# Kernel optimization log

Hardware: AMD Instinct MI355X
Metric: run time of the kernel (lower is better)

The kernel has to match this reference:

```python
import jax, jax.numpy as jnp
import numpy as np

B, D, K, V = 8192, 64, 200, 100000
EPS = 1e-5


def setup_inputs() -> dict:
    key = jax.random.key(0)
    ks = jax.random.split(key, 16)
    n = lambda k, s, sc=1.0: jax.random.normal(k, s, dtype=jnp.float32) * sc
    sw = 0.05  # weight scale for numeric stability
    inp = {
        'v_embed': n(ks[0], (V, D)),
        'embeds_u_1': n(ks[1], (B, D)),
        'embeds_u_2': n(ks[2], (B, D)),
        'embeds_u_3': n(ks[3], (B, D)),
        'embeds_u_4': n(ks[4], (B, D)),
        'embeds_v': n(ks[5], (B, D)),
        'w_ur1_w': n(ks[6], (D, D), sw), 'w_ur1_b': jnp.zeros((D,), jnp.float32),
        'w_ur2_w': n(ks[7], (D, D), sw), 'w_ur2_b': jnp.zeros((D,), jnp.float32),
        'w_vr1_w': n(ks[8], (D, D), sw), 'w_vr1_b': jnp.zeros((D,), jnp.float32),
        'w_vr2_w': n(ks[9], (D, D), sw), 'w_vr2_b': jnp.zeros((D,), jnp.float32),
        'w_uv1_w': n(ks[10], (2 * D, D), sw), 'w_uv1_b': jnp.zeros((D,), jnp.float32),
        'w_uv2_w': n(ks[11], (D, 16), sw), 'w_uv2_b': jnp.zeros((16,), jnp.float32),
        'w_uv3_w': n(ks[12], (16, 1), sw), 'w_uv3_b': jnp.zeros((1,), jnp.float32),
        'nodes_v': jax.random.randint(ks[13], (B,), 0, V),
        'nbr_idx': jax.random.randint(ks[14], (B, K), 0, V),
        'nbr_len': jax.random.randint(ks[15], (B,), 1, K),
    }
    for name, dim in (('bn1', D), ('bn2', D), ('bn3', D), ('bn4', 16)):
        inp[name + '_g'] = jnp.ones((dim,), jnp.float32)
        inp[name + '_b'] = jnp.zeros((dim,), jnp.float32)
        inp[name + '_m'] = jnp.zeros((dim,), jnp.float32)
        inp[name + '_v'] = jnp.ones((dim,), jnp.float32)
    return inp


def _bn(x, g, b, m, v):
    return (x - m) * jax.lax.rsqrt(v + EPS) * g + b


def reference(v_embed, embeds_u_1, embeds_u_2, embeds_u_3, embeds_u_4, embeds_v,
              w_ur1_w, w_ur1_b, w_ur2_w, w_ur2_b,
              w_vr1_w, w_vr1_b, w_vr2_w, w_vr2_b,
              w_uv1_w, w_uv1_b, w_uv2_w, w_uv2_b, w_uv3_w, w_uv3_b,
              bn1_g, bn1_b, bn1_m, bn1_v,
              bn2_g, bn2_b, bn2_m, bn2_v,
              bn3_g, bn3_b, bn3_m, bn3_v,
              bn4_g, bn4_b, bn4_m, bn4_v,
              nodes_v, nbr_idx, nbr_len):
    sg = jax.lax.stop_gradient
    # ragged nearest-neighbor min distance (torch used .data -> detached)
    ve = sg(v_embed)
    new_v = ve[nodes_v]                                    # [B, D]
    nbr = ve[nbr_idx]                                      # [B, K, D]
    d = jnp.sqrt(jnp.sum((new_v[:, None, :] - nbr) ** 2, axis=-1))  # [B, K]
    kk = nbr_idx.shape[1]
    mask = jnp.arange(kk)[None, :] < jnp.maximum(nbr_len, 1)[:, None]
    d_min = jnp.min(jnp.where(mask, d, jnp.inf), axis=1)   # [B]
    # per-sample curiosity c_u (detached in torch via .data)
    dist = lambda a, b: jnp.sqrt(jnp.sum((a - b) ** 2, axis=-1))
    u1, u2, u3, u4 = sg(embeds_u_1), sg(embeds_u_2), sg(embeds_u_3), sg(embeds_u_4)
    c = (dist(u1, u2) + dist(u2, u3) + dist(u3, u4)) / 3.0  # [B]
    # exponential-decay fusion of temporal user embeddings: e^-4..e^-1 / sum
    w = jnp.exp(-jnp.arange(4, 0, -1, dtype=jnp.float32))
    w = w / jnp.sum(w)
    embeds_u = (embeds_u_1 * w[0] + embeds_u_2 * w[1]
                + embeds_u_3 * w[2] + embeds_u_4 * w[3])
    # MLP head (eval mode: BN with running stats, dropout off)
    x_u = jax.nn.relu(_bn(embeds_u @ w_ur1_w + w_ur1_b, bn1_g, bn1_b, bn1_m, bn1_v))
    x_u = x_u @ w_ur2_w + w_ur2_b
    x_v = jax.nn.relu(_bn(embeds_v @ w_vr1_w + w_vr1_b, bn2_g, bn2_b, bn2_m, bn2_v))
    x_v = x_v @ w_vr2_w + w_vr2_b
    x = jnp.concatenate([x_u, x_v], axis=1)                # [B, 2D]
    x = jax.nn.relu(_bn(x @ w_uv1_w + w_uv1_b, bn3_g, bn3_b, bn3_m, bn3_v))
    x = jax.nn.relu(_bn(x @ w_uv2_w + w_uv2_b, bn4_g, bn4_b, bn4_m, bn4_v))
    scores = (x @ w_uv3_w + w_uv3_b)[:, 0]                 # [B]
    # unexpectedness term: batch min-max normalize, 6t*exp(-6t)
    t = (d_min - jnp.min(d_min)) / (jnp.max(d_min) - jnp.min(d_min))
    unexp = 6.0 * t * jnp.exp(-6.0 * t)
    cn = (c - jnp.min(c)) / (jnp.max(c) - jnp.min(c))
    return scores + unexp * cn
```

## Files before the change

kernel.cpp:

```cpp
#include <hip/hip_runtime.h>
#include <math.h>

#define NROWS 8192
#define DIM 64
#define KNBR 200
#define BN_EPS 1e-5f
#define BIGF 3.402823466e38f


__device__ __forceinline__ float matvec64(const float* xlds,
                                          const float* __restrict__ W,
                                          int lane) {
    float acc = 0.f;
#pragma unroll
    for (int i4 = 0; i4 < 16; ++i4) {
        float4 xv = *(const float4*)(xlds + i4 * 4);
        acc = fmaf(xv.x, W[(i4 * 4 + 0) * 64 + lane], acc);
        acc = fmaf(xv.y, W[(i4 * 4 + 1) * 64 + lane], acc);
        acc = fmaf(xv.z, W[(i4 * 4 + 2) * 64 + lane], acc);
        acc = fmaf(xv.w, W[(i4 * 4 + 3) * 64 + lane], acc);
    }
    return acc;
}

__device__ __forceinline__ float matvec128(const float* xlds,
                                           const float* __restrict__ W,
                                           int lane) {
    float acc = 0.f;
#pragma unroll
    for (int i4 = 0; i4 < 32; ++i4) {
        float4 xv = *(const float4*)(xlds + i4 * 4);
        acc = fmaf(xv.x, W[(i4 * 4 + 0) * 64 + lane], acc);
        acc = fmaf(xv.y, W[(i4 * 4 + 1) * 64 + lane], acc);
        acc = fmaf(xv.z, W[(i4 * 4 + 2) * 64 + lane], acc);
        acc = fmaf(xv.w, W[(i4 * 4 + 3) * 64 + lane], acc);
    }
    return acc;
}

__device__ __forceinline__ float d2part(const float4 a, const float4 b) {
    const float dx = a.x - b.x, dy = a.y - b.y, dz = a.z - b.z, dw = a.w - b.w;
    float d2 = dx * dx;
    d2 = fmaf(dy, dy, d2);
    d2 = fmaf(dz, dz, d2);
    d2 = fmaf(dw, dw, d2);
    return d2;
}

__device__ __forceinline__ float sum16(float v) {
    v += __shfl_xor(v, 1);
    v += __shfl_xor(v, 2);
    v += __shfl_xor(v, 4);
    v += __shfl_xor(v, 8);
    return v;
}

__global__ __launch_bounds__(256) void fused_rows(
    const float* __restrict__ v_embed,
    const float* __restrict__ u1p, const float* __restrict__ u2p,
    const float* __restrict__ u3p, const float* __restrict__ u4p,
    const float* __restrict__ evp,
    const float* __restrict__ w_ur1, const float* __restrict__ b_ur1,
    const float* __restrict__ w_ur2, const float* __restrict__ b_ur2,
    const float* __restrict__ w_vr1, const float* __restrict__ b_vr1,
    const float* __restrict__ w_vr2, const float* __restrict__ b_vr2,
    const float* __restrict__ w_uv1, const float* __restrict__ b_uv1,
    const float* __restrict__ w_uv2, const float* __restrict__ b_uv2,
    const float* __restrict__ w_uv3, const float* __restrict__ b_uv3,
    const float* __restrict__ bn1_g, const float* __restrict__ bn1_b,
    const float* __restrict__ bn1_m, const float* __restrict__ bn1_v,
    const float* __restrict__ bn2_g, const float* __restrict__ bn2_b,
    const float* __restrict__ bn2_m, const float* __restrict__ bn2_v,
    const float* __restrict__ bn3_g, const float* __restrict__ bn3_b,
    const float* __restrict__ bn3_m, const float* __restrict__ bn3_v,
    const float* __restrict__ bn4_g, const float* __restrict__ bn4_b,
    const float* __restrict__ bn4_m, const float* __restrict__ bn4_v,
    const int* __restrict__ nodes_v, const int* __restrict__ nbr_idx,
    const int* __restrict__ nbr_len,
    float* __restrict__ out_score, float* __restrict__ ws_d2,
    float* __restrict__ ws_c) {
    const int w = threadIdx.x >> 6;
    const int lane = threadIdx.x & 63;
    const int row = blockIdx.x * 4 + w;

    __shared__ float xbuf[4][132];

    const int l16 = lane & 15;
    const int g = lane >> 4;

    const int node = nodes_v[row];
    int len = nbr_len[row];
    if (len < 1) len = 1;
    const int lenm1 = len - 1;
    const float4 vq = ((const float4*)(v_embed + ((size_t)node << 6)))[l16];
    const int* nb = nbr_idx + (size_t)row * KNBR;

    float dmin2 = BIGF;
    for (int k0 = 0; k0 < len; k0 += 32) {
        int k[8];
#pragma unroll
        for (int j = 0; j < 8; ++j) {
            int kk = k0 + 4 * j + g;
            k[j] = kk < lenm1 ? kk : lenm1;
        }
        int idx[8];
#pragma unroll
        for (int j = 0; j < 8; ++j) idx[j] = nb[k[j]];
        float4 nv[8];
#pragma unroll
        for (int j = 0; j < 8; ++j) {
            nv[j] = ((const float4*)(v_embed + ((size_t)idx[j] << 6)))[l16];
        }
        float d[8];
#pragma unroll
        for (int j = 0; j < 8; ++j) d[j] = sum16(d2part(vq, nv[j]));
#pragma unroll
        for (int j = 0; j < 8; ++j) dmin2 = fminf(dmin2, d[j]);
    }
    dmin2 = fminf(dmin2, __shfl_xor(dmin2, 16));
    dmin2 = fminf(dmin2, __shfl_xor(dmin2, 32));

    float* xw = xbuf[w];
    const size_t rb = (size_t)row * DIM + lane;
    const float u1 = u1p[rb], u2 = u2p[rb], u3 = u3p[rb], u4 = u4p[rb];
    const float ev = evp[rb];

    float d12 = u1 - u2, d23 = u2 - u3, d34 = u3 - u4;
    float s1 = d12 * d12, s2 = d23 * d23, s3 = d34 * d34;
#pragma unroll
    for (int m = 1; m < 64; m <<= 1) {
        s1 += __shfl_xor(s1, m);
        s2 += __shfl_xor(s2, m);
        s3 += __shfl_xor(s3, m);
    }
    const float cval = (sqrtf(s1) + sqrtf(s2) + sqrtf(s3)) * (1.0f / 3.0f);

    float eu = u1 * 0.032058603280084993f;
    eu = fmaf(u2, 0.087144318742032567f, eu);
    eu = fmaf(u3, 0.236882818089910134f, eu);
    eu = fmaf(u4, 0.643914259887972245f, eu);

    xw[lane] = eu;
    float t1 = matvec64(xw, w_ur1, lane) + b_ur1[lane];
    t1 = (t1 - bn1_m[lane]) * rsqrtf(bn1_v[lane] + BN_EPS) * bn1_g[lane] + bn1_b[lane];
    t1 = fmaxf(t1, 0.f);
    xw[lane] = t1;
    const float xu = matvec64(xw, w_ur2, lane) + b_ur2[lane];
    xw[lane] = ev;
    float t2 = matvec64(xw, w_vr1, lane) + b_vr1[lane];
    t2 = (t2 - bn2_m[lane]) * rsqrtf(bn2_v[lane] + BN_EPS) * bn2_g[lane] + bn2_b[lane];
    t2 = fmaxf(t2, 0.f);
    xw[lane] = t2;
    const float xv = matvec64(xw, w_vr2, lane) + b_vr2[lane];
    xw[lane] = xu;
    xw[64 + lane] = xv;
    float t3 = matvec128(xw, w_uv1, lane) + b_uv1[lane];
    t3 = (t3 - bn3_m[lane]) * rsqrtf(bn3_v[lane] + BN_EPS) * bn3_g[lane] + bn3_b[lane];
    t3 = fmaxf(t3, 0.f);
    xw[lane] = t3;
    const int jj = lane & 15;
    const int q = lane >> 4;
    float h4 = 0.f;
#pragma unroll
    for (int i = 0; i < 16; ++i) {
        h4 = fmaf(xw[q * 16 + i], w_uv2[(q * 16 + i) * 16 + jj], h4);
    }
    h4 += __shfl_xor(h4, 16);
    h4 += __shfl_xor(h4, 32);
    h4 += b_uv2[jj];
    h4 = (h4 - bn4_m[jj]) * rsqrtf(bn4_v[jj] + BN_EPS) * bn4_g[jj] + bn4_b[jj];
    h4 = fmaxf(h4, 0.f);
    float p = h4 * w_uv3[jj];
#pragma unroll
    for (int m = 1; m < 16; m <<= 1) p += __shfl_xor(p, m);
    const float score = p + b_uv3[0];

    if (lane == 0) {
        out_score[row] = score;
        ws_d2[row] = dmin2;
        ws_c[row] = cval;
    }
}

__global__ __launch_bounds__(1024) void combine(
    const float* __restrict__ ws_d2, const float* __restrict__ ws_c,
    float* __restrict__ out) {
    const int tid = threadIdx.x;
    __shared__ float red[4][16];

    float ld2[8], lc[8];
    float dmin = BIGF, dmax = -BIGF, cmin = BIGF, cmax = -BIGF;
#pragma unroll
    for (int i = 0; i < 8; ++i) {
        const int b = tid * 8 + i;
        ld2[i] = ws_d2[b];
        lc[i] = ws_c[b];
        dmin = fminf(dmin, ld2[i]);
        dmax = fmaxf(dmax, ld2[i]);
        cmin = fminf(cmin, lc[i]);
        cmax = fmaxf(cmax, lc[i]);
    }
#pragma unroll
    for (int m = 1; m < 64; m <<= 1) {
        dmin = fminf(dmin, __shfl_xor(dmin, m));
        dmax = fmaxf(dmax, __shfl_xor(dmax, m));
        cmin = fminf(cmin, __shfl_xor(cmin, m));
        cmax = fmaxf(cmax, __shfl_xor(cmax, m));
    }
    const int wid = tid >> 6;
    const int lane = tid & 63;
    if (lane == 0) {
        red[0][wid] = dmin;
        red[1][wid] = dmax;
        red[2][wid] = cmin;
        red[3][wid] = cmax;
    }
    __syncthreads();
    dmin = red[0][0]; dmax = red[1][0]; cmin = red[2][0]; cmax = red[3][0];
#pragma unroll
    for (int i = 1; i < 16; ++i) {
        dmin = fminf(dmin, red[0][i]);
        dmax = fmaxf(dmax, red[1][i]);
        cmin = fminf(cmin, red[2][i]);
        cmax = fmaxf(cmax, red[3][i]);
    }
    const float dlo = sqrtf(dmin);
    const float dhi = sqrtf(dmax);
    const float inv_d = 1.f / (dhi - dlo);
    const float inv_c = 1.f / (cmax - cmin);
#pragma unroll
    for (int i = 0; i < 8; ++i) {
        const int b = tid * 8 + i;
        const float t = (sqrtf(ld2[i]) - dlo) * inv_d;
        const float unexp = 6.f * t * expf(-6.f * t);
        out[b] += unexp * (lc[i] - cmin) * inv_c;
    }
}

extern "C" void kernel_launch(void* const* d_in, const int* in_sizes, int n_in,
                              void* d_out, int out_size, void* d_ws, size_t ws_size,
                              hipStream_t stream) {
    const float* v_embed = (const float*)d_in[0];
    const float* u1 = (const float*)d_in[1];
    const float* u2 = (const float*)d_in[2];
    const float* u3 = (const float*)d_in[3];
    const float* u4 = (const float*)d_in[4];
    const float* ev = (const float*)d_in[5];
    const float* w_ur1 = (const float*)d_in[6];
    const float* b_ur1 = (const float*)d_in[7];
    const float* w_ur2 = (const float*)d_in[8];
    const float* b_ur2 = (const float*)d_in[9];
    const float* w_vr1 = (const float*)d_in[10];
    const float* b_vr1 = (const float*)d_in[11];
    const float* w_vr2 = (const float*)d_in[12];
    const float* b_vr2 = (const float*)d_in[13];
    const float* w_uv1 = (const float*)d_in[14];
    const float* b_uv1 = (const float*)d_in[15];
    const float* w_uv2 = (const float*)d_in[16];
    const float* b_uv2 = (const float*)d_in[17];
    const float* w_uv3 = (const float*)d_in[18];
    const float* b_uv3 = (const float*)d_in[19];
    const int* nodes_v = (const int*)d_in[20];
    const int* nbr_idx = (const int*)d_in[21];
    const int* nbr_len = (const int*)d_in[22];
    const float* bn1_g = (const float*)d_in[23];
    const float* bn1_b = (const float*)d_in[24];
    const float* bn1_m = (const float*)d_in[25];
    const float* bn1_v = (const float*)d_in[26];
    const float* bn2_g = (const float*)d_in[27];
    const float* bn2_b = (const float*)d_in[28];
    const float* bn2_m = (const float*)d_in[29];
    const float* bn2_v = (const float*)d_in[30];
    const float* bn3_g = (const float*)d_in[31];
    const float* bn3_b = (const float*)d_in[32];
    const float* bn3_m = (const float*)d_in[33];
    const float* bn3_v = (const float*)d_in[34];
    const float* bn4_g = (const float*)d_in[35];
    const float* bn4_b = (const float*)d_in[36];
    const float* bn4_m = (const float*)d_in[37];
    const float* bn4_v = (const float*)d_in[38];

    float* out = (float*)d_out;
    float* wsf = (float*)d_ws;
    float* ws_d2 = wsf;
    float* ws_c = wsf + NROWS;

    hipLaunchKernelGGL(fused_rows, dim3(NROWS / 4), dim3(256), 0, stream,
                       v_embed, u1, u2, u3, u4, ev,
                       w_ur1, b_ur1, w_ur2, b_ur2, w_vr1, b_vr1, w_vr2, b_vr2,
                       w_uv1, b_uv1, w_uv2, b_uv2, w_uv3, b_uv3,
                       bn1_g, bn1_b, bn1_m, bn1_v,
                       bn2_g, bn2_b, bn2_m, bn2_v,
                       bn3_g, bn3_b, bn3_m, bn3_v,
                       bn4_g, bn4_b, bn4_m, bn4_v,
                       nodes_v, nbr_idx, nbr_len,
                       out, ws_d2, ws_c);
    hipLaunchKernelGGL(combine, dim3(1), dim3(1024), 0, stream,
                       ws_d2, ws_c, out);
}
```

Baseline: 62.00 us.

## Split neighbor-distance search into per-row blocks separate from MLP blocks

The kernel grid is split in two. The first NROWS blocks each handle one row's nearest-neighbor search, with four waves covering 64 neighbors each, all gathers issued at once, and a 4-lane shuffle reduction. The remaining blocks run the MLP head with four rows per block, as before. This is meant to expose far more memory-level parallelism for the latency-bound random gathers and to remove the serial loop over neighbors. In exchange it launches many more blocks, adds a block-level barrier per row, and wastes waves whose 64-neighbor chunk lies beyond the row's length.

```diff
diff --git a/kernel.cpp b/kernel.cpp
--- a/kernel.cpp
+++ b/kernel.cpp
@@ -47,15 +47,7 @@
     return d2;
 }
 
-__device__ __forceinline__ float sum16(float v) {
-    v += __shfl_xor(v, 1);
-    v += __shfl_xor(v, 2);
-    v += __shfl_xor(v, 4);
-    v += __shfl_xor(v, 8);
-    return v;
-}
-
-__global__ __launch_bounds__(256) void fused_rows(
+__global__ __launch_bounds__(256, 4) void fused_main(
     const float* __restrict__ v_embed,
     const float* __restrict__ u1p, const float* __restrict__ u2p,
     const float* __restrict__ u3p, const float* __restrict__ u4p,
@@ -81,45 +73,67 @@
     float* __restrict__ ws_c) {
     const int w = threadIdx.x >> 6;
     const int lane = threadIdx.x & 63;
-    const int row = blockIdx.x * 4 + w;
 
     __shared__ float xbuf[4][132];
-
-    const int l16 = lane & 15;
-    const int g = lane >> 4;
-
-    const int node = nodes_v[row];
-    int len = nbr_len[row];
-    if (len < 1) len = 1;
-    const int lenm1 = len - 1;
-    const float4 vq = ((const float4*)(v_embed + ((size_t)node << 6)))[l16];
-    const int* nb = nbr_idx + (size_t)row * KNBR;
-
-    float dmin2 = BIGF;
-    for (int k0 = 0; k0 < len; k0 += 32) {
-        int k[8];
-#pragma unroll
-        for (int j = 0; j < 8; ++j) {
-            int kk = k0 + 4 * j + g;
-            k[j] = kk < lenm1 ? kk : lenm1;
+    __shared__ float pr[4];
+
+    if (blockIdx.x < NROWS) {
+        const int row = blockIdx.x;
+        int len = nbr_len[row];
+        if (len < 1) len = 1;
+        const int c = w;
+        float dmin2 = BIGF;
+        if (c * 64 < len) {
+            const int lenm1 = len - 1;
+            const int q16 = lane >> 2;
+            const int sub = lane & 3;
+            const int node = nodes_v[row];
+            const float4* vrow = (const float4*)(v_embed + ((size_t)node << 6));
+            const float4 q0 = vrow[sub + 0];
+            const float4 q1 = vrow[sub + 4];
+            const float4 q2 = vrow[sub + 8];
+            const float4 q3 = vrow[sub + 12];
+            const int* nb = nbr_idx + (size_t)row * KNBR;
+            const int base = c * 64 + q16;
+            int n0 = base;           n0 = n0 < lenm1 ? n0 : lenm1;
+            int n1 = base + 16;      n1 = n1 < lenm1 ? n1 : lenm1;
+            int n2 = base + 32;      n2 = n2 < lenm1 ? n2 : lenm1;
+            int n3 = base + 48;      n3 = n3 < lenm1 ? n3 : lenm1;
+            const int i0 = nb[n0];
+            const int i1 = nb[n1];
+            const int i2 = nb[n2];
+            const int i3 = nb[n3];
+            const float4* r0 = (const float4*)(v_embed + ((size_t)i0 << 6));
+            const float4* r1 = (const float4*)(v_embed + ((size_t)i1 << 6));
+            const float4* r2 = (const float4*)(v_embed + ((size_t)i2 << 6));
+            const float4* r3 = (const float4*)(v_embed + ((size_t)i3 << 6));
+            const float4 a00 = r0[sub + 0], a01 = r0[sub + 4], a02 = r0[sub + 8], a03 = r0[sub + 12];
+            const float4 a10 = r1[sub + 0], a11 = r1[sub + 4], a12 = r1[sub + 8], a13 = r1[sub + 12];
+            const float4 a20 = r2[sub + 0], a21 = r2[sub + 4], a22 = r2[sub + 8], a23 = r2[sub + 12];
+            const float4 a30 = r3[sub + 0], a31 = r3[sub + 4], a32 = r3[sub + 8], a33 = r3[sub + 12];
+            float d0 = d2part(q0, a00) + d2part(q1, a01) + d2part(q2, a02) + d2part(q3, a03);
+            float d1 = d2part(q0, a10) + d2part(q1, a11) + d2part(q2, a12) + d2part(q3, a13);
+            float d2 = d2part(q0, a20) + d2part(q1, a21) + d2part(q2, a22) + d2part(q3, a23);
+            float d3 = d2part(q0, a30) + d2part(q1, a31) + d2part(q2, a32) + d2part(q3, a33);
+            d0 += __shfl_xor(d0, 1); d0 += __shfl_xor(d0, 2);
+            d1 += __shfl_xor(d1, 1); d1 += __shfl_xor(d1, 2);
+            d2 += __shfl_xor(d2, 1); d2 += __shfl_xor(d2, 2);
+            d3 += __shfl_xor(d3, 1); d3 += __shfl_xor(d3, 2);
+            dmin2 = fminf(fminf(d0, d1), fminf(d2, d3));
         }
-        int idx[8];
-#pragma unroll
-        for (int j = 0; j < 8; ++j) idx[j] = nb[k[j]];
-        float4 nv[8];
-#pragma unroll
-        for (int j = 0; j < 8; ++j) {
-            nv[j] = ((const float4*)(v_embed + ((size_t)idx[j] << 6)))[l16];
+        dmin2 = fminf(dmin2, __shfl_xor(dmin2, 4));
+        dmin2 = fminf(dmin2, __shfl_xor(dmin2, 8));
+        dmin2 = fminf(dmin2, __shfl_xor(dmin2, 16));
+        dmin2 = fminf(dmin2, __shfl_xor(dmin2, 32));
+        if (lane == 0) pr[w] = dmin2;
+        __syncthreads();
+        if (threadIdx.x == 0) {
+            ws_d2[row] = fminf(fminf(pr[0], pr[1]), fminf(pr[2], pr[3]));
         }
-        float d[8];
-#pragma unroll
-        for (int j = 0; j < 8; ++j) d[j] = sum16(d2part(vq, nv[j]));
-#pragma unroll
-        for (int j = 0; j < 8; ++j) dmin2 = fminf(dmin2, d[j]);
-    }
-    dmin2 = fminf(dmin2, __shfl_xor(dmin2, 16));
-    dmin2 = fminf(dmin2, __shfl_xor(dmin2, 32));
-
+        return;
+    }
+
+    const int row = (blockIdx.x - NROWS) * 4 + w;
     float* xw = xbuf[w];
     const size_t rb = (size_t)row * DIM + lane;
     const float u1 = u1p[rb], u2 = u2p[rb], u3 = u3p[rb], u4 = u4p[rb];
@@ -177,7 +191,6 @@
 
     if (lane == 0) {
         out_score[row] = score;
-        ws_d2[row] = dmin2;
         ws_c[row] = cval;
     }
 }
@@ -285,7 +298,7 @@
     float* ws_d2 = wsf;
     float* ws_c = wsf + NROWS;
 
-    hipLaunchKernelGGL(fused_rows, dim3(NROWS / 4), dim3(256), 0, stream,
+    hipLaunchKernelGGL(fused_main, dim3(NROWS + NROWS / 4), dim3(256), 0, stream,
                        v_embed, u1, u2, u3, u4, ev,
                        w_ur1, b_ur1, w_ur2, b_ur2, w_vr1, b_vr1, w_vr2, b_vr2,
                        w_uv1, b_uv1, w_uv2, b_uv2, w_uv3, b_uv3,
```

After: 63.28 us. 2.1% more time.

## Bin neighbor indices by table slice to localize embedding gathers

Applied to the files above, without the earlier changes.

Adds a pre-pass kernel that partitions each row's neighbor indices into 8 slices of the embedding table. The main kernel then runs one block per (row-group, slice), so blocks that run at the same time gather from a smaller region of v_embed, aiming for better L2/MALL locality. Partial minima are written per slice and reduced in the combine kernel. The cost is an extra kernel launch, workspace traffic for the binned lists, and many more small blocks with little work per slice.

```diff
diff --git a/kernel.cpp b/kernel.cpp
--- a/kernel.cpp
+++ b/kernel.cpp
@@ -4,6 +4,8 @@
 #define NROWS 8192
 #define DIM 64
 #define KNBR 200
+#define NSLICE 8
+#define SLICE_ROWS 12500
 #define BN_EPS 1e-5f
 #define BIGF 3.402823466e38f
 
@@ -47,15 +49,57 @@
     return d2;
 }
 
-__device__ __forceinline__ float sum16(float v) {
-    v += __shfl_xor(v, 1);
-    v += __shfl_xor(v, 2);
-    v += __shfl_xor(v, 4);
-    v += __shfl_xor(v, 8);
-    return v;
-}
-
-__global__ __launch_bounds__(256) void fused_rows(
+__global__ __launch_bounds__(256) void bin_rows(
+    const int* __restrict__ nbr_idx, const int* __restrict__ nbr_len,
+    int* __restrict__ ws_list, int* __restrict__ ws_cnt,
+    int* __restrict__ ws_off) {
+    const int w = threadIdx.x >> 6;
+    const int lane = threadIdx.x & 63;
+    const int row = blockIdx.x * 4 + w;
+
+    __shared__ int cnt[4][NSLICE];
+    __shared__ int off[4][NSLICE];
+
+    if (lane < NSLICE) cnt[w][lane] = 0;
+    __syncthreads();
+
+    int len = nbr_len[row];
+    if (len < 1) len = 1;
+    const int* nb = nbr_idx + (size_t)row * KNBR;
+
+    int myidx[4], myslice[4], mypos[4];
+#pragma unroll
+    for (int t = 0; t < 4; ++t) {
+        const int k = t * 64 + lane;
+        const bool v = k < len;
+        const int idx = v ? nb[k] : 0;
+        const int s = idx / SLICE_ROWS;
+        myidx[t] = idx;
+        myslice[t] = s;
+        mypos[t] = v ? atomicAdd(&cnt[w][s], 1) : 0;
+    }
+    __syncthreads();
+    if (lane == 0) {
+        int acc = 0;
+#pragma unroll
+        for (int s = 0; s < NSLICE; ++s) { off[w][s] = acc; acc += cnt[w][s]; }
+    }
+    __syncthreads();
+#pragma unroll
+    for (int t = 0; t < 4; ++t) {
+        const int k = t * 64 + lane;
+        if (k < len) {
+            ws_list[(size_t)row * KNBR + off[w][myslice[t]] + mypos[t]] = myidx[t];
+        }
+    }
+    if (lane < NSLICE) {
+        ws_cnt[row * NSLICE + lane] = cnt[w][lane];
+        ws_off[row * NSLICE + lane] = off[w][lane];
+    }
+}
+
+#define GATHER_BLOCKS (NROWS / 4 * NSLICE)
+__global__ __launch_bounds__(256) void fused_main(
     const float* __restrict__ v_embed,
     const float* __restrict__ u1p, const float* __restrict__ u2p,
     const float* __restrict__ u3p, const float* __restrict__ u4p,
@@ -75,51 +119,57 @@
     const float* __restrict__ bn3_m, const float* __restrict__ bn3_v,
     const float* __restrict__ bn4_g, const float* __restrict__ bn4_b,
     const float* __restrict__ bn4_m, const float* __restrict__ bn4_v,
-    const int* __restrict__ nodes_v, const int* __restrict__ nbr_idx,
-    const int* __restrict__ nbr_len,
-    float* __restrict__ out_score, float* __restrict__ ws_d2,
+    const int* __restrict__ nodes_v, const int* __restrict__ nbr_len,
+    const int* __restrict__ ws_list, const int* __restrict__ ws_cnt,
+    const int* __restrict__ ws_off,
+    float* __restrict__ out_score, float* __restrict__ ws_d2p,
     float* __restrict__ ws_c) {
     const int w = threadIdx.x >> 6;
     const int lane = threadIdx.x & 63;
-    const int row = blockIdx.x * 4 + w;
 
     __shared__ float xbuf[4][132];
 
-    const int l16 = lane & 15;
-    const int g = lane >> 4;
-
-    const int node = nodes_v[row];
-    int len = nbr_len[row];
-    if (len < 1) len = 1;
-    const int lenm1 = len - 1;
-    const float4 vq = ((const float4*)(v_embed + ((size_t)node << 6)))[l16];
-    const int* nb = nbr_idx + (size_t)row * KNBR;
-
-    float dmin2 = BIGF;
-    for (int k0 = 0; k0 < len; k0 += 32) {
-        int k[8];
-#pragma unroll
-        for (int j = 0; j < 8; ++j) {
-            int kk = k0 + 4 * j + g;
-            k[j] = kk < lenm1 ? kk : lenm1;
+    if (blockIdx.x < GATHER_BLOCKS) {
+        const int s = blockIdx.x & 7;
+        const int row = (blockIdx.x >> 3) * 4 + w;
+        const int cnt = ws_cnt[row * NSLICE + s];
+        float dmin2 = BIGF;
+        if (cnt > 0) {
+            const int off = ws_off[row * NSLICE + s];
+            const int q16 = lane >> 2;
+            const int sub = lane & 3;
+            const int node = nodes_v[row];
+            const float4* vrow = (const float4*)(v_embed + ((size_t)node << 6));
+            const float4 q0 = vrow[sub + 0];
+            const float4 q1 = vrow[sub + 4];
+            const float4 q2 = vrow[sub + 8];
+            const float4 q3 = vrow[sub + 12];
+            const int* lst = ws_list + (size_t)row * KNBR + off;
+            const int cm1 = cnt - 1;
+            for (int j0 = 0; j0 < cnt; j0 += 16) {
+                int j = j0 + q16;
+                j = j < cm1 ? j : cm1;
+                const int idx = lst[j];
+                const float4* r = (const float4*)(v_embed + ((size_t)idx << 6));
+                const float4 a0 = r[sub + 0];
+                const float4 a1 = r[sub + 4];
+                const float4 a2 = r[sub + 8];
+                const float4 a3 = r[sub + 12];
+                float d = d2part(q0, a0) + d2part(q1, a1) + d2part(q2, a2) + d2part(q3, a3);
+                d += __shfl_xor(d, 1);
+                d += __shfl_xor(d, 2);
+                dmin2 = fminf(dmin2, d);
+            }
         }
-        int idx[8];
-#pragma unroll
-        for (int j = 0; j < 8; ++j) idx[j] = nb[k[j]];
-        float4 nv[8];
-#pragma unroll
-        for (int j = 0; j < 8; ++j) {
-            nv[j] = ((const float4*)(v_embed + ((size_t)idx[j] << 6)))[l16];
-        }
-        float d[8];
-#pragma unroll
-        for (int j = 0; j < 8; ++j) d[j] = sum16(d2part(vq, nv[j]));
-#pragma unroll
-        for (int j = 0; j < 8; ++j) dmin2 = fminf(dmin2, d[j]);
-    }
-    dmin2 = fminf(dmin2, __shfl_xor(dmin2, 16));
-    dmin2 = fminf(dmin2, __shfl_xor(dmin2, 32));
-
+        dmin2 = fminf(dmin2, __shfl_xor(dmin2, 4));
+        dmin2 = fminf(dmin2, __shfl_xor(dmin2, 8));
+        dmin2 = fminf(dmin2, __shfl_xor(dmin2, 16));
+        dmin2 = fminf(dmin2, __shfl_xor(dmin2, 32));
+        if (lane == 0) ws_d2p[row * NSLICE + s] = dmin2;
+        return;
+    }
+
+    const int row = (blockIdx.x - GATHER_BLOCKS) * 4 + w;
     float* xw = xbuf[w];
     const size_t rb = (size_t)row * DIM + lane;
     const float u1 = u1p[rb], u2 = u2p[rb], u3 = u3p[rb], u4 = u4p[rb];
@@ -177,13 +227,12 @@
 
     if (lane == 0) {
         out_score[row] = score;
-        ws_d2[row] = dmin2;
         ws_c[row] = cval;
     }
 }
 
 __global__ __launch_bounds__(1024) void combine(
-    const float* __restrict__ ws_d2, const float* __restrict__ ws_c,
+    const float* __restrict__ ws_d2p, const float* __restrict__ ws_c,
     float* __restrict__ out) {
     const int tid = threadIdx.x;
     __shared__ float red[4][16];
@@ -193,10 +242,13 @@
 #pragma unroll
     for (int i = 0; i < 8; ++i) {
         const int b = tid * 8 + i;
-        ld2[i] = ws_d2[b];
+        float m = ws_d2p[b * NSLICE];
+#pragma unroll
+        for (int s = 1; s < NSLICE; ++s) m = fminf(m, ws_d2p[b * NSLICE + s]);
+        ld2[i] = m;
         lc[i] = ws_c[b];
-        dmin = fminf(dmin, ld2[i]);
-        dmax = fmaxf(dmax, ld2[i]);
+        dmin = fminf(dmin, m);
+        dmax = fmaxf(dmax, m);
         cmin = fminf(cmin, lc[i]);
         cmax = fmaxf(cmax, lc[i]);
     }
@@ -281,11 +333,15 @@
     const float* bn4_v = (const float*)d_in[38];
 
     float* out = (float*)d_out;
-    float* wsf = (float*)d_ws;
-    float* ws_d2 = wsf;
-    float* ws_c = wsf + NROWS;
-
-    hipLaunchKernelGGL(fused_rows, dim3(NROWS / 4), dim3(256), 0, stream,
+    int* ws_list = (int*)d_ws;
+    int* ws_cnt = ws_list + (size_t)NROWS * KNBR;
+    int* ws_off = ws_cnt + NROWS * NSLICE;
+    float* ws_d2p = (float*)(ws_off + NROWS * NSLICE);
+    float* ws_c = ws_d2p + NROWS * NSLICE;
+
+    hipLaunchKernelGGL(bin_rows, dim3(NROWS / 4), dim3(256), 0, stream,
+                       nbr_idx, nbr_len, ws_list, ws_cnt, ws_off);
+    hipLaunchKernelGGL(fused_main, dim3(GATHER_BLOCKS + NROWS / 4), dim3(256), 0, stream,
                        v_embed, u1, u2, u3, u4, ev,
                        w_ur1, b_ur1, w_ur2, b_ur2, w_vr1, b_vr1, w_vr2, b_vr2,
                        w_uv1, b_uv1, w_uv2, b_uv2, w_uv3, b_uv3,
@@ -293,8 +349,8 @@
                        bn2_g, bn2_b, bn2_m, bn2_v,
                        bn3_g, bn3_b, bn3_m, bn3_v,
                        bn4_g, bn4_b, bn4_m, bn4_v,
-                       nodes_v, nbr_idx, nbr_len,
-                       out, ws_d2, ws_c);
+                       nodes_v, nbr_len, ws_list, ws_cnt, ws_off,
+                       out, ws_d2p, ws_c);
     hipLaunchKernelGGL(combine, dim3(1), dim3(1024), 0, stream,
-                       ws_d2, ws_c, out);
-}
+                       ws_d2p, ws_c, out);
+}
```

After: 86.02 us. +38.7%, slower.
